# Kernel tuning notes

Hardware: AMD Instinct MI355X
Metric: run time of the kernel (lower is better)

Reference implementation:

```python
import jax, jax.numpy as jnp
import numpy as np

N_NODES = 50000
N_EDGES = 800000
N_FEAT, N_HID, N_LATENT = 512, 256, 128


def spmm(rows, cols, vals, dense):
    # out[r] += vals[e] * dense[cols[e]]  -- COO SpMM via segment_sum
    gathered = dense[cols] * vals[:, None]          # [E, d]
    return jax.ops.segment_sum(gathered, rows, num_segments=N_NODES)


def setup_inputs() -> dict:
    key = jax.random.key(0)
    ks = jax.random.split(key, 8)
    x = jax.random.normal(ks[0], (N_NODES, N_FEAT), dtype=jnp.float32)
    edge_rows = jax.random.randint(ks[1], (N_EDGES,), 0, N_NODES, dtype=jnp.int32)
    edge_cols = jax.random.randint(ks[2], (N_EDGES,), 0, N_NODES, dtype=jnp.int32)
    edge_vals = jax.random.uniform(ks[3], (N_EDGES,), dtype=jnp.float32)
    # Glorot-style init like the torch GraphConvolution
    W1 = jax.random.normal(ks[4], (N_FEAT, N_HID), dtype=jnp.float32) / np.sqrt(N_FEAT)
    b1 = jnp.zeros((N_HID,), dtype=jnp.float32)
    W2 = jax.random.normal(ks[5], (N_HID, N_LATENT), dtype=jnp.float32) / np.sqrt(N_HID)
    b2 = jnp.zeros((N_LATENT,), dtype=jnp.float32)
    return {"x": x, "edge_rows": edge_rows, "edge_cols": edge_cols,
            "edge_vals": edge_vals, "W1": W1, "b1": b1, "W2": W2, "b2": b2}


def reference(x, edge_rows, edge_cols, edge_vals, W1, b1, W2, b2):
    # layer 1: relu(adj @ (x @ W1) + b1)
    h = spmm(edge_rows, edge_cols, edge_vals, x @ W1) + b1
    h = jax.nn.relu(h)
    # layer 2: relu(adj @ (h @ W2) + b2)
    z = spmm(edge_rows, edge_cols, edge_vals, h @ W2) + b2
    return jax.nn.relu(z)
```

## Files before the change

### kernel.cpp

```cpp
#include <hip/hip_runtime.h>
#include <hip/hip_bf16.h>


typedef __attribute__((ext_vector_type(8))) short bf16x8;
typedef __attribute__((ext_vector_type(4))) float f32x4;

#define NN 50000
#define NE 800000
#define NF 512
#define NH 256
#define NL 128
#define NB ((NN + 255) / 256)

static __device__ __forceinline__ unsigned short f2bf(float f) {
  union { float f; unsigned int u; } v; v.f = f;
  unsigned int r = v.u + 0x7fffu + ((v.u >> 16) & 1u);
  return (unsigned short)(r >> 16);
}
static __device__ __forceinline__ float bf2f(unsigned short u) {
  union { unsigned int u; float f; } v; v.u = (unsigned int)u << 16;
  return v.f;
}

extern "C" __global__ void k_hist(const int* __restrict__ rows, int* __restrict__ counts, int n) {
  int i = blockIdx.x * 256 + threadIdx.x;
  if (i < n) atomicAdd(&counts[rows[i]], 1);
}

extern "C" __global__ __launch_bounds__(256) void k_blocksum(
    const int* __restrict__ counts, int* __restrict__ bsum, int n) {
  __shared__ int s[256];
  int t = threadIdx.x;
  int i = blockIdx.x * 256 + t;
  s[t] = (i < n) ? counts[i] : 0;
  __syncthreads();
  for (int off = 128; off > 0; off >>= 1) {
    if (t < off) s[t] += s[t + off];
    __syncthreads();
  }
  if (t == 0) bsum[blockIdx.x] = s[0];
}

extern "C" __global__ __launch_bounds__(256) void k_scansums(
    const int* __restrict__ bsum, int* __restrict__ bpre, int* __restrict__ rp, int nb, int n) {
  __shared__ int s[256];
  int t = threadIdx.x;
  int v = (t < nb) ? bsum[t] : 0;
  s[t] = v;
  __syncthreads();
  for (int off = 1; off < 256; off <<= 1) {
    int u = (t >= off) ? s[t - off] : 0;
    __syncthreads();
    s[t] += u;
    __syncthreads();
  }
  if (t < nb) bpre[t] = s[t] - v;
  if (t == 255) rp[n] = s[255];
}

extern "C" __global__ __launch_bounds__(256) void k_scanfin(
    const int* __restrict__ counts, const int* __restrict__ bpre,
    int* __restrict__ rp, int* __restrict__ cur, int n) {
  __shared__ int s[256];
  int t = threadIdx.x;
  int i = blockIdx.x * 256 + t;
  int c = (i < n) ? counts[i] : 0;
  s[t] = c;
  __syncthreads();
  for (int off = 1; off < 256; off <<= 1) {
    int u = (t >= off) ? s[t - off] : 0;
    __syncthreads();
    s[t] += u;
    __syncthreads();
  }
  if (i < n) {
    int e = bpre[blockIdx.x] + s[t] - c;
    rp[i] = e;
    cur[i] = e;
  }
}

extern "C" __global__ void k_scatter(const int* __restrict__ rows, const int* __restrict__ cols,
    const float* __restrict__ vals, int* __restrict__ cur,
    int* __restrict__ scol, float* __restrict__ sval, int n) {
  int i = blockIdx.x * 256 + threadIdx.x;
  if (i < n) {
    int p = atomicAdd(&cur[rows[i]], 1);
    scol[p] = cols[i];
    sval[p] = vals[i];
  }
}

extern "C" __global__ void k_cast4(const float4* __restrict__ in, ushort4* __restrict__ out, int n4) {
  int i = blockIdx.x * 256 + threadIdx.x;
  if (i < n4) {
    float4 f = in[i];
    ushort4 o; o.x = f2bf(f.x); o.y = f2bf(f.y); o.z = f2bf(f.z); o.w = f2bf(f.w);
    out[i] = o;
  }
}

extern "C" __global__ void k_transcast(const float* __restrict__ w, unsigned short* __restrict__ wt,
                                       int K, int N) {
  int k = blockIdx.x; int n = threadIdx.x;
  wt[(size_t)n * K + k] = f2bf(w[(size_t)k * N + n]);
}

#define BM 128
#define BN 128
#define BK 32

extern "C" __global__ __launch_bounds__(256) void k_gemm(
    const unsigned short* __restrict__ A, const unsigned short* __restrict__ BT,
    unsigned short* __restrict__ C, int M, int N, int K) {
  __shared__ __align__(16) unsigned short sA[BM * BK];
  __shared__ __align__(16) unsigned short sB[BN * BK];
  int tid = threadIdx.x;
  int lane = tid & 63, wid = tid >> 6;
  int wm = (wid >> 1) * 64, wn = (wid & 1) * 64;
  int bm = blockIdx.x * BM, bn = blockIdx.y * BN;
  int l15 = lane & 15, lq = lane >> 4;
  f32x4 acc[4][4];
#pragma unroll
  for (int i = 0; i < 4; ++i)
#pragma unroll
    for (int j = 0; j < 4; ++j) acc[i][j] = (f32x4){0.f, 0.f, 0.f, 0.f};

  for (int k0 = 0; k0 < K; k0 += BK) {
#pragma unroll
    for (int i = 0; i < 2; ++i) {
      int u = tid + 256 * i;
      int row = u >> 2, uc = (u & 3) * 8;
      int ga = bm + row; if (ga >= M) ga = M - 1;
      *(float4*)(&sA[row * BK + uc]) = *(const float4*)(A + (size_t)ga * K + k0 + uc);
      int gb = bn + row; if (gb >= N) gb = N - 1;
      *(float4*)(&sB[row * BK + uc]) = *(const float4*)(BT + (size_t)gb * K + k0 + uc);
    }
    __syncthreads();
    bf16x8 af[4], bfr[4];
#pragma unroll
    for (int t = 0; t < 4; ++t) {
      af[t]  = *(const bf16x8*)(&sA[(wm + t * 16 + l15) * BK + lq * 8]);
      bfr[t] = *(const bf16x8*)(&sB[(wn + t * 16 + l15) * BK + lq * 8]);
    }
#pragma unroll
    for (int mt = 0; mt < 4; ++mt)
#pragma unroll
      for (int nt = 0; nt < 4; ++nt)
        acc[mt][nt] = __builtin_amdgcn_mfma_f32_16x16x32_bf16(af[mt], bfr[nt], acc[mt][nt], 0, 0, 0);
    __syncthreads();
  }
#pragma unroll
  for (int mt = 0; mt < 4; ++mt) {
#pragma unroll
    for (int r = 0; r < 4; ++r) {
      int gr = bm + wm + mt * 16 + lq * 4 + r;
      if (gr < M) {
#pragma unroll
        for (int nt = 0; nt < 4; ++nt) {
          int gc = bn + wn + nt * 16 + l15;
          C[(size_t)gr * N + gc] = f2bf(acc[mt][nt][r]);
        }
      }
    }
  }
}

extern "C" __global__ __launch_bounds__(256) void k_spmm256(
    const int* __restrict__ rp, const int* __restrict__ scol, const float* __restrict__ sval,
    const unsigned short* __restrict__ src, const float* __restrict__ bias,
    ushort4* __restrict__ out) {
  int row = blockIdx.x * 4 + (threadIdx.x >> 6);
  int lane = threadIdx.x & 63;
  if (row >= NN) return;
  int e0 = __builtin_amdgcn_readfirstlane(rp[row]);
  int e1 = __builtin_amdgcn_readfirstlane(rp[row + 1]);
  const ushort4* srcv = (const ushort4*)src;
  float4 acc = {0.f, 0.f, 0.f, 0.f};
  for (int e = e0; e < e1; ++e) {
    int c = scol[e];
    float v = sval[e];
    ushort4 g = srcv[(size_t)c * (NH / 4) + lane];
    acc.x = fmaf(v, bf2f(g.x), acc.x);
    acc.y = fmaf(v, bf2f(g.y), acc.y);
    acc.z = fmaf(v, bf2f(g.z), acc.z);
    acc.w = fmaf(v, bf2f(g.w), acc.w);
  }
  float4 b = ((const float4*)bias)[lane];
  ushort4 o;
  o.x = f2bf(fmaxf(acc.x + b.x, 0.f));
  o.y = f2bf(fmaxf(acc.y + b.y, 0.f));
  o.z = f2bf(fmaxf(acc.z + b.z, 0.f));
  o.w = f2bf(fmaxf(acc.w + b.w, 0.f));
  out[(size_t)row * (NH / 4) + lane] = o;
}

extern "C" __global__ __launch_bounds__(256) void k_spmm128(
    const int* __restrict__ rp, const int* __restrict__ scol, const float* __restrict__ sval,
    const unsigned short* __restrict__ src, const float* __restrict__ bias,
    float2* __restrict__ out) {
  int row = blockIdx.x * 4 + (threadIdx.x >> 6);
  int lane = threadIdx.x & 63;
  if (row >= NN) return;
  int e0 = __builtin_amdgcn_readfirstlane(rp[row]);
  int e1 = __builtin_amdgcn_readfirstlane(rp[row + 1]);
  const ushort2* srcv = (const ushort2*)src;
  float2 acc = {0.f, 0.f};
  for (int e = e0; e < e1; ++e) {
    int c = scol[e];
    float v = sval[e];
    ushort2 g = srcv[(size_t)c * (NL / 2) + lane];
    acc.x = fmaf(v, bf2f(g.x), acc.x);
    acc.y = fmaf(v, bf2f(g.y), acc.y);
  }
  float2 b = ((const float2*)bias)[lane];
  float2 o;
  o.x = fmaxf(acc.x + b.x, 0.f);
  o.y = fmaxf(acc.y + b.y, 0.f);
  out[(size_t)row * (NL / 2) + lane] = o;
}

extern "C" void kernel_launch(void* const* d_in, const int* in_sizes, int n_in,
                              void* d_out, int out_size, void* d_ws, size_t ws_size,
                              hipStream_t stream) {
  const float* x   = (const float*)d_in[0];
  const int* erow  = (const int*)d_in[1];
  const int* ecol  = (const int*)d_in[2];
  const float* ev  = (const float*)d_in[3];
  const float* W1  = (const float*)d_in[4];
  const float* b1  = (const float*)d_in[5];
  const float* W2  = (const float*)d_in[6];
  const float* b2  = (const float*)d_in[7];

  char* ws = (char*)d_ws;
  unsigned short* xbf = (unsigned short*)(ws + 0);
  unsigned short* xwb = (unsigned short*)(ws + 51200000);
  unsigned short* hbf = (unsigned short*)(ws + 76800000);
  unsigned short* hwb = (unsigned short*)(ws + 102400000);
  unsigned short* w1t = (unsigned short*)(ws + 115200000);
  unsigned short* w2t = (unsigned short*)(ws + 115462144);
  int* rp    = (int*)(ws + 115527680);
  int* cur   = (int*)(ws + 115728384);
  int* cnt   = (int*)(ws + 115929088);
  int* bsum  = (int*)(ws + 116129792);
  int* bpre  = (int*)(ws + 116130816);
  int* scol  = (int*)(ws + 116131840);
  float* sval = (float*)(ws + 119331840);

  hipMemsetAsync(cnt, 0, NN * sizeof(int), stream);
  k_hist<<<NE / 256, 256, 0, stream>>>(erow, cnt, NE);
  k_blocksum<<<NB, 256, 0, stream>>>(cnt, bsum, NN);
  k_scansums<<<1, 256, 0, stream>>>(bsum, bpre, rp, NB, NN);
  k_scanfin<<<NB, 256, 0, stream>>>(cnt, bpre, rp, cur, NN);
  k_scatter<<<NE / 256, 256, 0, stream>>>(erow, ecol, ev, cur, scol, sval, NE);

  k_cast4<<<(NN * NF / 4) / 256, 256, 0, stream>>>((const float4*)x, (ushort4*)xbf, NN * NF / 4);
  k_transcast<<<NF, NH, 0, stream>>>(W1, w1t, NF, NH);
  k_gemm<<<dim3((NN + BM - 1) / BM, NH / BN), 256, 0, stream>>>(xbf, w1t, xwb, NN, NH, NF);
  k_spmm256<<<NN / 4, 256, 0, stream>>>(rp, scol, sval, xwb, b1, (ushort4*)hbf);

  k_transcast<<<NH, NL, 0, stream>>>(W2, w2t, NH, NL);
  k_gemm<<<dim3((NN + BM - 1) / BM, NL / BN), 256, 0, stream>>>(hbf, w2t, hwb, NN, NL, NH);
  k_spmm128<<<NN / 4, 256, 0, stream>>>(rp, scol, sval, hwb, b2, (float2*)d_out);
}
```

Baseline: 434.7 us.

## Pack CSR edges as int2, unroll SpMM gathers, and use direct global-to-LDS loads in GEMM

Column index and value are interleaved into one int2 array, so each edge in the SpMM kernels needs one load instead of two separate streams. Both SpMM kernels unroll the edge loop by four so that four row gathers are in flight at once. The GEMM fills its shared tiles with global_load_lds instead of loading through registers. The edge-interleaving and unrolling target gather latency and fewer memory instructions. The LDS path depends on the builtin's layout semantics (per-lane 16-byte writes to LDS) being correct on this target.

```diff
diff --git a/kernel.cpp b/kernel.cpp
--- a/kernel.cpp
+++ b/kernel.cpp
@@ -20,6 +20,12 @@
 static __device__ __forceinline__ float bf2f(unsigned short u) {
   union { unsigned int u; float f; } v; v.u = (unsigned int)u << 16;
   return v.f;
+}
+
+static __device__ __forceinline__ void gll16(const void* g, void* l) {
+  __builtin_amdgcn_global_load_lds(
+      (const __attribute__((address_space(1))) void*)g,
+      (__attribute__((address_space(3))) void*)l, 16, 0, 0);
 }
 
 extern "C" __global__ void k_hist(const int* __restrict__ rows, int* __restrict__ counts, int n) {
@@ -81,13 +87,12 @@
 }
 
 extern "C" __global__ void k_scatter(const int* __restrict__ rows, const int* __restrict__ cols,
-    const float* __restrict__ vals, int* __restrict__ cur,
-    int* __restrict__ scol, float* __restrict__ sval, int n) {
+    const float* __restrict__ vals, int* __restrict__ cur, int2* __restrict__ ep, int n) {
   int i = blockIdx.x * 256 + threadIdx.x;
   if (i < n) {
     int p = atomicAdd(&cur[rows[i]], 1);
-    scol[p] = cols[i];
-    sval[p] = vals[i];
+    int2 e; e.x = cols[i]; e.y = __float_as_int(vals[i]);
+    ep[p] = e;
   }
 }
 
@@ -132,9 +137,9 @@
       int u = tid + 256 * i;
       int row = u >> 2, uc = (u & 3) * 8;
       int ga = bm + row; if (ga >= M) ga = M - 1;
-      *(float4*)(&sA[row * BK + uc]) = *(const float4*)(A + (size_t)ga * K + k0 + uc);
+      gll16(A + (size_t)ga * K + k0 + uc, &sA[row * BK + uc]);
       int gb = bn + row; if (gb >= N) gb = N - 1;
-      *(float4*)(&sB[row * BK + uc]) = *(const float4*)(BT + (size_t)gb * K + k0 + uc);
+      gll16(BT + (size_t)gb * K + k0 + uc, &sB[row * BK + uc]);
     }
     __syncthreads();
     bf16x8 af[4], bfr[4];
@@ -167,7 +172,7 @@
 }
 
 extern "C" __global__ __launch_bounds__(256) void k_spmm256(
-    const int* __restrict__ rp, const int* __restrict__ scol, const float* __restrict__ sval,
+    const int* __restrict__ rp, const int2* __restrict__ ep,
     const unsigned short* __restrict__ src, const float* __restrict__ bias,
     ushort4* __restrict__ out) {
   int row = blockIdx.x * 4 + (threadIdx.x >> 6);
@@ -177,14 +182,30 @@
   int e1 = __builtin_amdgcn_readfirstlane(rp[row + 1]);
   const ushort4* srcv = (const ushort4*)src;
   float4 acc = {0.f, 0.f, 0.f, 0.f};
-  for (int e = e0; e < e1; ++e) {
-    int c = scol[e];
-    float v = sval[e];
-    ushort4 g = srcv[(size_t)c * (NH / 4) + lane];
-    acc.x = fmaf(v, bf2f(g.x), acc.x);
-    acc.y = fmaf(v, bf2f(g.y), acc.y);
-    acc.z = fmaf(v, bf2f(g.z), acc.z);
-    acc.w = fmaf(v, bf2f(g.w), acc.w);
+  int e = e0;
+  for (; e + 4 <= e1; e += 4) {
+    int2 p0 = ep[e], p1 = ep[e + 1], p2 = ep[e + 2], p3 = ep[e + 3];
+    ushort4 g0 = srcv[(size_t)p0.x * (NH / 4) + lane];
+    ushort4 g1 = srcv[(size_t)p1.x * (NH / 4) + lane];
+    ushort4 g2 = srcv[(size_t)p2.x * (NH / 4) + lane];
+    ushort4 g3 = srcv[(size_t)p3.x * (NH / 4) + lane];
+    float v0 = __int_as_float(p0.y), v1 = __int_as_float(p1.y);
+    float v2 = __int_as_float(p2.y), v3 = __int_as_float(p3.y);
+    acc.x = fmaf(v0, bf2f(g0.x), acc.x); acc.y = fmaf(v0, bf2f(g0.y), acc.y);
+    acc.z = fmaf(v0, bf2f(g0.z), acc.z); acc.w = fmaf(v0, bf2f(g0.w), acc.w);
+    acc.x = fmaf(v1, bf2f(g1.x), acc.x); acc.y = fmaf(v1, bf2f(g1.y), acc.y);
+    acc.z = fmaf(v1, bf2f(g1.z), acc.z); acc.w = fmaf(v1, bf2f(g1.w), acc.w);
+    acc.x = fmaf(v2, bf2f(g2.x), acc.x); acc.y = fmaf(v2, bf2f(g2.y), acc.y);
+    acc.z = fmaf(v2, bf2f(g2.z), acc.z); acc.w = fmaf(v2, bf2f(g2.w), acc.w);
+    acc.x = fmaf(v3, bf2f(g3.x), acc.x); acc.y = fmaf(v3, bf2f(g3.y), acc.y);
+    acc.z = fmaf(v3, bf2f(g3.z), acc.z); acc.w = fmaf(v3, bf2f(g3.w), acc.w);
+  }
+  for (; e < e1; ++e) {
+    int2 p = ep[e];
+    float v = __int_as_float(p.y);
+    ushort4 g = srcv[(size_t)p.x * (NH / 4) + lane];
+    acc.x = fmaf(v, bf2f(g.x), acc.x); acc.y = fmaf(v, bf2f(g.y), acc.y);
+    acc.z = fmaf(v, bf2f(g.z), acc.z); acc.w = fmaf(v, bf2f(g.w), acc.w);
   }
   float4 b = ((const float4*)bias)[lane];
   ushort4 o;
@@ -196,7 +217,7 @@
 }
 
 extern "C" __global__ __launch_bounds__(256) void k_spmm128(
-    const int* __restrict__ rp, const int* __restrict__ scol, const float* __restrict__ sval,
+    const int* __restrict__ rp, const int2* __restrict__ ep,
     const unsigned short* __restrict__ src, const float* __restrict__ bias,
     float2* __restrict__ out) {
   int row = blockIdx.x * 4 + (threadIdx.x >> 6);
@@ -206,12 +227,25 @@
   int e1 = __builtin_amdgcn_readfirstlane(rp[row + 1]);
   const ushort2* srcv = (const ushort2*)src;
   float2 acc = {0.f, 0.f};
-  for (int e = e0; e < e1; ++e) {
-    int c = scol[e];
-    float v = sval[e];
-    ushort2 g = srcv[(size_t)c * (NL / 2) + lane];
-    acc.x = fmaf(v, bf2f(g.x), acc.x);
-    acc.y = fmaf(v, bf2f(g.y), acc.y);
+  int e = e0;
+  for (; e + 4 <= e1; e += 4) {
+    int2 p0 = ep[e], p1 = ep[e + 1], p2 = ep[e + 2], p3 = ep[e + 3];
+    ushort2 g0 = srcv[(size_t)p0.x * (NL / 2) + lane];
+    ushort2 g1 = srcv[(size_t)p1.x * (NL / 2) + lane];
+    ushort2 g2 = srcv[(size_t)p2.x * (NL / 2) + lane];
+    ushort2 g3 = srcv[(size_t)p3.x * (NL / 2) + lane];
+    float v0 = __int_as_float(p0.y), v1 = __int_as_float(p1.y);
+    float v2 = __int_as_float(p2.y), v3 = __int_as_float(p3.y);
+    acc.x = fmaf(v0, bf2f(g0.x), acc.x); acc.y = fmaf(v0, bf2f(g0.y), acc.y);
+    acc.x = fmaf(v1, bf2f(g1.x), acc.x); acc.y = fmaf(v1, bf2f(g1.y), acc.y);
+    acc.x = fmaf(v2, bf2f(g2.x), acc.x); acc.y = fmaf(v2, bf2f(g2.y), acc.y);
+    acc.x = fmaf(v3, bf2f(g3.x), acc.x); acc.y = fmaf(v3, bf2f(g3.y), acc.y);
+  }
+  for (; e < e1; ++e) {
+    int2 p = ep[e];
+    float v = __int_as_float(p.y);
+    ushort2 g = srcv[(size_t)p.x * (NL / 2) + lane];
+    acc.x = fmaf(v, bf2f(g.x), acc.x); acc.y = fmaf(v, bf2f(g.y), acc.y);
   }
   float2 b = ((const float2*)bias)[lane];
   float2 o;
@@ -244,22 +278,21 @@
   int* cnt   = (int*)(ws + 115929088);
   int* bsum  = (int*)(ws + 116129792);
   int* bpre  = (int*)(ws + 116130816);
-  int* scol  = (int*)(ws + 116131840);
-  float* sval = (float*)(ws + 119331840);
+  int2* ep   = (int2*)(ws + 116131840);
 
   hipMemsetAsync(cnt, 0, NN * sizeof(int), stream);
   k_hist<<<NE / 256, 256, 0, stream>>>(erow, cnt, NE);
   k_blocksum<<<NB, 256, 0, stream>>>(cnt, bsum, NN);
   k_scansums<<<1, 256, 0, stream>>>(bsum, bpre, rp, NB, NN);
   k_scanfin<<<NB, 256, 0, stream>>>(cnt, bpre, rp, cur, NN);
-  k_scatter<<<NE / 256, 256, 0, stream>>>(erow, ecol, ev, cur, scol, sval, NE);
+  k_scatter<<<NE / 256, 256, 0, stream>>>(erow, ecol, ev, cur, ep, NE);
 
   k_cast4<<<(NN * NF / 4) / 256, 256, 0, stream>>>((const float4*)x, (ushort4*)xbf, NN * NF / 4);
   k_transcast<<<NF, NH, 0, stream>>>(W1, w1t, NF, NH);
   k_gemm<<<dim3((NN + BM - 1) / BM, NH / BN), 256, 0, stream>>>(xbf, w1t, xwb, NN, NH, NF);
-  k_spmm256<<<NN / 4, 256, 0, stream>>>(rp, scol, sval, xwb, b1, (ushort4*)hbf);
+  k_spmm256<<<NN / 4, 256, 0, stream>>>(rp, ep, xwb, b1, (ushort4*)hbf);
 
   k_transcast<<<NH, NL, 0, stream>>>(W2, w2t, NH, NL);
   k_gemm<<<dim3((NN + BM - 1) / BM, NL / BN), 256, 0, stream>>>(hbf, w2t, hwb, NN, NL, NH);
-  k_spmm128<<<NN / 4, 256, 0, stream>>>(rp, scol, sval, hwb, b2, (float2*)d_out);
-}
+  k_spmm128<<<NN / 4, 256, 0, stream>>>(rp, ep, hwb, b2, (float2*)d_out);
+}
```

Result: faster. 397.6 us (-8.5%).
